# Optimization experiments

Measured on AMD Instinct MI355X. Metric: run time of the kernel, lower is better.

Reference implementation:

```python
import jax, jax.numpy as jnp
import numpy as np

B, N, D, E, H = 8, 256, 128, 32, 4
HD = D // H
EPS = 1e-5


def setup_inputs() -> dict:
    key = jax.random.key(0)
    ks = jax.random.split(key, 20)
    idx = jnp.arange(N)

    h = jax.random.normal(ks[0], (B, N, D), dtype=jnp.float32)
    adj = (jax.random.uniform(ks[1], (B, N, N)) < 0.5).astype(jnp.float32)
    adj = adj.at[:, idx, idx].set(1.0)
    edge_features = jax.random.normal(ks[2], (B, N, N, E), dtype=jnp.float32)
    src_mask = (jax.random.uniform(ks[3], (B, N, N)) < 0.7).astype(jnp.float32)
    src_mask = src_mask.at[:, idx, idx].set(1.0)

    s = 1.0 / np.sqrt(D)
    se = 1.0 / np.sqrt(E)
    p = {
        "gcn_w": jax.random.normal(ks[4], (D, D)) * s,
        "gcn_b": jnp.zeros((D,)),
        "edge_w": jax.random.normal(ks[5], (D, E)) * se,
        "edge_b": jnp.zeros((D,)),
        "wq": jax.random.normal(ks[6], (D, D)) * s,
        "wk": jax.random.normal(ks[7], (D, D)) * s,
        "wv": jax.random.normal(ks[8], (D, D)) * s,
        "bq": jnp.zeros((D,)),
        "bk": jnp.zeros((D,)),
        "bv": jnp.zeros((D,)),
        "out_w": jax.random.normal(ks[9], (D, D)) * s,
        "out_b": jnp.zeros((D,)),
        "ln_g": jnp.ones((D,)),
        "ln_b": jnp.zeros((D,)),
    }
    return {"h": h, "adj": adj, "edge_features": edge_features, "src_mask": src_mask, **p}


def reference(h, adj, edge_features, src_mask,
              gcn_w, gcn_b, edge_w, edge_b,
              wq, wk, wv, bq, bk, bv, out_w, out_b, ln_g, ln_b):
    b, n, d = h.shape

    # --- GCN branch: degree-normalized aggregation with self-loops ---
    adj_sl = adj + jnp.eye(n, dtype=h.dtype)[None]          # (B,N,N)
    deg = adj_sl.sum(-1, keepdims=True)                      # (B,N,1)
    h_agg = jnp.einsum('bnm,bmd->bnd', adj_sl, h) / deg
    h_gcn = h_agg @ gcn_w.T + gcn_b                          # (B,N,D)

    # --- edge-conditioned key/value: h_ij = h_j + edge_emb ---
    edge_emb = jnp.einsum('bnme,de->bnmd', edge_features, edge_w) + edge_b
    h_ij = h[:, None, :, :] + edge_emb                       # (B,N,N,D)

    # key padding mask: True where edge absent (masked)
    masked = (adj * src_mask) == 0                           # (B,N,N)

    # --- multi-head attention, one query per node ---
    q = (h @ wq.T + bq).reshape(b, n, H, HD)                 # (B,N,H,HD)
    k = (jnp.einsum('bnmd,ed->bnme', h_ij, wk) + bk).reshape(b, n, n, H, HD)
    v = (jnp.einsum('bnmd,ed->bnme', h_ij, wv) + bv).reshape(b, n, n, H, HD)

    scores = jnp.einsum('bnhd,bnmhd->bnhm', q, k) / np.sqrt(HD)  # (B,N,H,N)
    scores = jnp.where(masked[:, :, None, :], -jnp.inf, scores)
    attn = jax.nn.softmax(scores, axis=-1)
    o = jnp.einsum('bnhm,bnmhd->bnhd', attn, v).reshape(b, n, d)
    o = o @ out_w.T + out_b                                  # (B,N,D)

    # residual + layernorm (dropout is identity in eval)
    x = h + o
    mu = x.mean(-1, keepdims=True)
    var = ((x - mu) ** 2).mean(-1, keepdims=True)
    h_attn = ln_g * (x - mu) / jnp.sqrt(var + EPS) + ln_b

    return h_gcn + h_attn
```

## Files before the change

### kernel.cpp

```cpp
#include <hip/hip_runtime.h>
#include <hip/hip_bf16.h>

#define OFF_WQT 0
#define OFF_WKT 16384
#define OFF_WVT 32768
#define OFF_OWT 49152
#define OFF_GWT 65536
#define OFF_WKE 81920
#define OFF_WVET 86016
#define OFF_KB  90112
#define OFF_VB  90240
#define OFF_SC  90368
#define OFF_QSP 98560
#define OFF_QEP 229632
#define OFF_HG  360704
#define OFF_K0P 622848
#define OFF_V0P 753920

using half2_t = __attribute__((ext_vector_type(2))) __fp16;

static __device__ __forceinline__ half2_t u2h(unsigned int u){
  union { unsigned int u; half2_t h; } x; x.u = u; return x.h;
}
static __device__ __forceinline__ unsigned int pkf16(float a, float b){
  union { half2_t h; unsigned int u; } x;
  x.h = __builtin_amdgcn_cvt_pkrtz(a, b);
  return x.u;
}
static __device__ __forceinline__ float fdot2(unsigned int a, unsigned int b, float c){
  return __builtin_amdgcn_fdot2(u2h(a), u2h(b), c, false);
}

__global__ __launch_bounds__(256) void prep_kernel(
    const float* __restrict__ wq, const float* __restrict__ wk,
    const float* __restrict__ wv, const float* __restrict__ out_w,
    const float* __restrict__ gcn_w, const float* __restrict__ edge_w,
    const float* __restrict__ edge_b, const float* __restrict__ bk,
    const float* __restrict__ bv, float* __restrict__ ws)
{
  int blk = blockIdx.x, t = threadIdx.x;
  if (blk < 320) {
    int w = blk >> 6;
    int e0 = (blk & 63) * 256 + t;
    const float* src = (w==0) ? wq : (w==1) ? wk : (w==2) ? wv : (w==3) ? out_w : gcn_w;
    float* dst = ws + ((w==0) ? OFF_WQT : (w==1) ? OFF_WKT : (w==2) ? OFF_WVT
                      : (w==3) ? OFF_OWT : OFF_GWT);
    int k = e0 >> 7, d = e0 & 127;
    dst[e0] = src[d*128 + k];
  } else if (blk < 352) {
    int idx = blk - 320;
    int which = idx >> 4;
    int e0 = (idx & 15) * 256 + t;
    int dd = e0 >> 5, e = e0 & 31;
    const float* W = which ? wv : wk;
    float acc = 0.f;
    #pragma unroll 4
    for (int k2 = 0; k2 < 128; ++k2) acc += W[dd*128+k2] * edge_w[k2*32+e];
    if (which) ws[OFF_WVET + e*128 + dd] = acc;
    else       ws[OFF_WKE + e0] = acc;
  } else {
    int dd = t & 127;
    const float* W  = (t < 128) ? wk : wv;
    const float* bb = (t < 128) ? bk : bv;
    float acc = bb[dd];
    #pragma unroll 4
    for (int k2 = 0; k2 < 128; ++k2) acc += W[dd*128+k2] * edge_b[k2];
    ws[((t < 128) ? OFF_KB : OFF_VB) + dd] = acc;
  }
}

__global__ __launch_bounds__(256) void proj_kernel(
    const float* __restrict__ h, const float* __restrict__ adj,
    const float* __restrict__ bq, const float* __restrict__ gcn_b,
    float* __restrict__ ws)
{
  __shared__ float h_lds[256];
  __shared__ float adj_lds[512];
  __shared__ float p1[2][2][128];
  __shared__ float p2[2][2][128];
  __shared__ float p3[2][2][128];
  __shared__ float qrow[2*132];
  __shared__ float qe_l[2*132];
  __shared__ float dpart[2][2];
  __shared__ float ha_lds[2*132];

  int t = threadIdx.x;
  int d = t & 127, kh = t >> 7;
  int r0 = blockIdx.x * 2;
  int b  = r0 >> 8, n0 = r0 & 255;
  unsigned int* wsu = (unsigned int*)ws;

  if (t < 64)  ((float4*)h_lds)[t]   = ((const float4*)(h   + (size_t)r0*128))[t];
  if (t < 128) ((float4*)adj_lds)[t] = ((const float4*)(adj + (size_t)r0*256))[t];
  __syncthreads();

  {
    const float* wqT = ws + OFF_WQT;
    const float* wkT = ws + OFF_WKT;
    const float* wvT = ws + OFF_WVT;
    float aq0=0,aq1=0,ak0=0,ak1=0,av0=0,av1=0;
    #pragma unroll 4
    for (int kk = 0; kk < 64; ++kk) {
      int k = kh*64 + kk;
      float qw = wqT[k*128+d], kw = wkT[k*128+d], vw = wvT[k*128+d];
      float h0 = h_lds[k], h1 = h_lds[128+k];
      aq0 += qw*h0; aq1 += qw*h1;
      ak0 += kw*h0; ak1 += kw*h1;
      av0 += vw*h0; av1 += vw*h1;
    }
    p1[kh][0][d]=aq0; p1[kh][1][d]=aq1;
    p2[kh][0][d]=ak0; p2[kh][1][d]=ak1;
    p3[kh][0][d]=av0; p3[kh][1][d]=av1;
  }
  __syncthreads();

  {
    int i = t >> 7, dd = t & 127;
    const float inv = 0.17677669529663687f;
    qrow[i*132 + dd] = (p1[0][i][dd] + p1[1][i][dd] + bq[dd]) * inv;
  }
  {
    int i = (t >> 6) & 1, pr = t & 63;
    if (t < 128) {
      float k0 = p2[0][i][2*pr] + p2[1][i][2*pr];
      float k1 = p2[0][i][2*pr+1] + p2[1][i][2*pr+1];
      wsu[OFF_K0P + (size_t)(r0+i)*64 + pr] = pkf16(k0, k1);
    } else {
      float v0 = p3[0][i][2*pr] + p3[1][i][2*pr];
      float v1 = p3[0][i][2*pr+1] + p3[1][i][2*pr+1];
      wsu[OFF_V0P + (size_t)(r0+i)*64 + pr] = pkf16(v0, v1);
    }
  }
  __syncthreads();

  if (t < 128) {
    int i = t >> 6, pr = t & 63;
    wsu[OFF_QSP + (size_t)(r0+i)*64 + pr] = pkf16(qrow[i*132 + 2*pr], qrow[i*132 + 2*pr+1]);
  }
  {
    int i = t >> 7, he = t & 127, hh = he >> 5, e = he & 31;
    float acc = 0.f;
    #pragma unroll
    for (int j = 0; j < 32; ++j)
      acc += ws[OFF_WKE + (hh*32 + j)*32 + e] * qrow[i*132 + hh*32 + j];
    qe_l[i*132 + he] = acc;
  }
  if (t < 8) {
    int i = t >> 2, hh = t & 3;
    float acc = 0.f;
    #pragma unroll
    for (int j = 0; j < 32; ++j)
      acc += qrow[i*132 + hh*32 + j] * ws[OFF_KB + hh*32 + j];
    ws[OFF_SC + (size_t)(r0+i)*4 + hh] = acc;
  }
  {
    float ag0=0, ag1=0, dg0=0, dg1=0;
    #pragma unroll 4
    for (int mm = 0; mm < 128; ++mm) {
      int ml = kh*128 + mm;
      float hv = h[((size_t)b*256 + ml)*128 + d];
      float a0 = adj_lds[ml]       + ((ml == n0)     ? 1.0f : 0.0f);
      float a1 = adj_lds[256 + ml] + ((ml == n0 + 1) ? 1.0f : 0.0f);
      ag0 += a0*hv; ag1 += a1*hv; dg0 += a0; dg1 += a1;
    }
    p1[kh][0][d]=ag0; p1[kh][1][d]=ag1;
    if (d == 0) { dpart[kh][0]=dg0; dpart[kh][1]=dg1; }
  }
  __syncthreads();

  if (t < 128) {
    int i = t >> 6, pr = t & 63;
    wsu[OFF_QEP + (size_t)(r0+i)*64 + pr] = pkf16(qe_l[i*132 + 2*pr], qe_l[i*132 + 2*pr+1]);
  }
  {
    int i = t >> 7, dd = t & 127;
    ha_lds[i*132 + dd] = (p1[0][i][dd] + p1[1][i][dd]) / (dpart[0][i] + dpart[1][i]);
  }
  __syncthreads();

  {
    const float* gwT = ws + OFF_GWT;
    float g0=0, g1=0;
    #pragma unroll 4
    for (int kk = 0; kk < 64; ++kk) {
      int k = kh*64 + kk;
      float gw = gwT[k*128+d];
      g0 += gw * ha_lds[k];
      g1 += gw * ha_lds[132 + k];
    }
    p2[kh][0][d]=g0; p2[kh][1][d]=g1;
  }
  __syncthreads();
  {
    int i = t >> 7, dd = t & 127;
    ws[OFF_HG + (size_t)(r0+i)*128 + dd] = p2[0][i][dd] + p2[1][i][dd] + gcn_b[dd];
  }
}

__global__ __launch_bounds__(256, 5) void attn_kernel(
    const float* __restrict__ edge, const float* __restrict__ adj,
    const float* __restrict__ srcm, const float* __restrict__ h,
    const float* __restrict__ out_b, const float* __restrict__ ln_g,
    const float* __restrict__ ln_b, const float* __restrict__ ws,
    float* __restrict__ out)
{
  __shared__ unsigned int e_lds[256*18];
  __shared__ float s_buf[4*264];
  __shared__ float part4[8*132];
  __shared__ float part5[8*132];
  __shared__ float wpart[16];

  float* const s_lds = s_buf;
  float* const eb_l  = s_buf;
  float* const o_l   = s_buf + 132;
  float* const px    = s_buf + 264;
  float* const stat  = s_buf + 520;

  const int t  = threadIdx.x;
  const int bn = blockIdx.x;
  const int b  = bn >> 8;
  const int hh = t & 3;
  const int mq = t >> 2;
  const unsigned int* wsu = (const unsigned int*)ws;

  const float4* et = (const float4*)(edge + (size_t)bn*8192);

  float4 va = et[t];
  float4 vb = et[256 + t];
  float mp_my = adj[(size_t)bn*256 + t] * srcm[(size_t)bn*256 + t];

  unsigned int qs_pk[16], qe_pk[16];
  {
    const uint4* qp = (const uint4*)(wsu + OFF_QSP + (size_t)bn*64 + hh*16);
    const uint4* qe = (const uint4*)(wsu + OFF_QEP + (size_t)bn*64 + hh*16);
    #pragma unroll
    for (int j = 0; j < 4; ++j) {
      uint4 a = qp[j];
      qs_pk[4*j+0]=a.x; qs_pk[4*j+1]=a.y; qs_pk[4*j+2]=a.z; qs_pk[4*j+3]=a.w;
      uint4 c = qe[j];
      qe_pk[4*j+0]=c.x; qe_pk[4*j+1]=c.y; qe_pk[4*j+2]=c.z; qe_pk[4*j+3]=c.w;
    }
  }
  float sconst = ws[OFF_SC + (size_t)bn*4 + hh];
  const unsigned int* K0 = wsu + OFF_K0P + (size_t)b*256*64;

  float exacc = 0.f;
  #pragma unroll
  for (int c = 0; c < 4; ++c) {
    {
      int fi = c*512 + t;
      int row = fi >> 3, c4 = fi & 7;
      uint2 pk;
      pk.x = pkf16(va.x, va.y);
      pk.y = pkf16(va.z, va.w);
      *(uint2*)(e_lds + row*18 + c4*2) = pk;
      int fj = fi + 256;
      int row2 = fj >> 3, c42 = fj & 7;
      uint2 pk2;
      pk2.x = pkf16(vb.x, vb.y);
      pk2.y = pkf16(vb.z, vb.w);
      *(uint2*)(e_lds + row2*18 + c42*2) = pk2;
    }
    if (c == 0) e_lds[t*18 + 16] = __float_as_uint(mp_my);
    if (c < 3) {
      va = et[(c+1)*512 + t];
      vb = et[(c+1)*512 + 256 + t];
    }
    __syncthreads();

    int mm = (c << 6) | mq;
    float acc = sconst;
    const uint4* kr4 = (const uint4*)(K0 + (size_t)mm*64 + hh*16);
    #pragma unroll
    for (int j4 = 0; j4 < 4; ++j4) {
      uint4 kw = kr4[j4];
      acc = fdot2(qs_pk[4*j4+0], kw.x, acc);
      acc = fdot2(qs_pk[4*j4+1], kw.y, acc);
      acc = fdot2(qs_pk[4*j4+2], kw.z, acc);
      acc = fdot2(qs_pk[4*j4+3], kw.w, acc);
    }
    const uint2* er = (const uint2*)(e_lds + mm*18);
    #pragma unroll
    for (int j2 = 0; j2 < 8; ++j2) {
      uint2 w = er[j2];
      acc = fdot2(qe_pk[2*j2+0], w.x, acc);
      acc = fdot2(qe_pk[2*j2+1], w.y, acc);
    }
    float mp = __uint_as_float(e_lds[mm*18 + 16]);
    float ex = (mp == 0.0f) ? 0.0f : __expf(acc);
    s_lds[hh*264 + mm] = ex;
    exacc += ex;
  }
  exacc += __shfl_down(exacc, 4);
  exacc += __shfl_down(exacc, 8);
  exacc += __shfl_down(exacc, 16);
  exacc += __shfl_down(exacc, 32);
  if ((t & 63) < 4) wpart[(t >> 6)*4 + hh] = exacc;
  __syncthreads();

  {
    int ms  = t >> 5;
    int hh4 = (t >> 3) & 3, e4 = t & 7;
    int c   = t & 31,  hh5 = c >> 3;
    float p4x=0,p4y=0,p4z=0,p4w=0;
    float p5x=0,p5y=0,p5z=0,p5w=0;
    const unsigned int* vrow = wsu + OFF_V0P + (size_t)b*256*64;
    for (int jm = 0; jm < 32; ++jm) {
      int mm = ms*32 + jm;
      float a4 = s_lds[hh4*264 + mm];
      uint2 w = *(const uint2*)(e_lds + mm*18 + e4*2);
      half2_t e0 = u2h(w.x), e1 = u2h(w.y);
      p4x += a4*(float)e0.x; p4y += a4*(float)e0.y;
      p4z += a4*(float)e1.x; p4w += a4*(float)e1.y;
      float a5 = s_lds[hh5*264 + mm];
      uint2 vv = *(const uint2*)(vrow + (size_t)mm*64 + c*2);
      half2_t v0 = u2h(vv.x), v1 = u2h(vv.y);
      p5x += a5*(float)v0.x; p5y += a5*(float)v0.y;
      p5z += a5*(float)v1.x; p5w += a5*(float)v1.y;
    }
    float4 f4; f4.x=p4x; f4.y=p4y; f4.z=p4z; f4.w=p4w;
    *(float4*)(part4 + ms*132 + hh4*32 + e4*4) = f4;
    float4 f5; f5.x=p5x; f5.y=p5y; f5.z=p5z; f5.w=p5w;
    *(float4*)(part5 + ms*132 + c*4) = f5;
  }
  __syncthreads();

  float ov_reg = 0.f;
  if (t < 128) {
    int ht = t >> 5;
    float inv = 1.0f / (wpart[ht] + wpart[4+ht] + wpart[8+ht] + wpart[12+ht]);
    float se = 0.f, s2 = 0.f;
    #pragma unroll
    for (int g = 0; g < 8; ++g) { se += part4[g*132 + t]; s2 += part5[g*132 + t]; }
    eb_l[t] = se * inv;
    ov_reg  = s2 * inv;
  }
  __syncthreads();

  if (t < 128) {
    int hd = t >> 5;
    float acc = ov_reg + ws[OFF_VB + t];
    const float* wveT = ws + OFF_WVET;
    #pragma unroll 4
    for (int e = 0; e < 32; ++e) acc += wveT[e*128 + t] * eb_l[hd*32 + e];
    o_l[t] = acc;
  }
  __syncthreads();

  {
    int d = t & 127, kh = t >> 7;
    const float* owT = ws + OFF_OWT;
    float xa = 0.f;
    #pragma unroll 4
    for (int kk = 0; kk < 64; ++kk) {
      int k = kh*64 + kk;
      xa += owT[k*128 + d] * o_l[k];
    }
    px[kh*128 + d] = xa;
  }
  __syncthreads();

  float x = 0.f;
  if (t < 128) {
    x = px[t] + px[128 + t] + out_b[t] + h[(size_t)bn*128 + t];
    float s = x, ss = x*x;
    #pragma unroll
    for (int off = 32; off > 0; off >>= 1) {
      s  += __shfl_down(s,  off);
      ss += __shfl_down(ss, off);
    }
    if ((t & 63) == 0) { stat[t >> 6] = s; stat[2 + (t >> 6)] = ss; }
  }
  __syncthreads();

  if (t < 128) {
    float mu   = (stat[0] + stat[1]) * (1.0f/128.0f);
    float var  = (stat[2] + stat[3]) * (1.0f/128.0f) - mu*mu;
    float rstd = rsqrtf(var + 1e-5f);
    out[(size_t)bn*128 + t] =
        ln_g[t]*(x - mu)*rstd + ln_b[t] + ws[OFF_HG + (size_t)bn*128 + t];
  }
}

extern "C" void kernel_launch(void* const* d_in, const int* in_sizes, int n_in,
                              void* d_out, int out_size, void* d_ws, size_t ws_size,
                              hipStream_t stream) {
  (void)in_sizes; (void)n_in; (void)out_size; (void)ws_size;
  const float* h     = (const float*)d_in[0];
  const float* adj   = (const float*)d_in[1];
  const float* edge  = (const float*)d_in[2];
  const float* srcm  = (const float*)d_in[3];
  const float* gcn_w = (const float*)d_in[4];
  const float* gcn_b = (const float*)d_in[5];
  const float* edge_w= (const float*)d_in[6];
  const float* edge_b= (const float*)d_in[7];
  const float* wq    = (const float*)d_in[8];
  const float* wk    = (const float*)d_in[9];
  const float* wv    = (const float*)d_in[10];
  const float* bq    = (const float*)d_in[11];
  const float* bk    = (const float*)d_in[12];
  const float* bv    = (const float*)d_in[13];
  const float* out_w = (const float*)d_in[14];
  const float* out_b = (const float*)d_in[15];
  const float* ln_g  = (const float*)d_in[16];
  const float* ln_b  = (const float*)d_in[17];

  float* ws  = (float*)d_ws;
  float* out = (float*)d_out;

  prep_kernel<<<353, 256, 0, stream>>>(wq, wk, wv, out_w, gcn_w, edge_w, edge_b, bk, bv, ws);
  proj_kernel<<<1024, 256, 0, stream>>>(h, adj, bq, gcn_b, ws);
  attn_kernel<<<2048, 256, 0, stream>>>(edge, adj, srcm, h, out_b, ln_g, ln_b, ws, out);
}
```

Measured before the change: 185.4 us.

## Stream edge chunks through double-buffered LDS and fuse weighted sums per chunk

Replaces the full 256-row edge LDS tile and the partial-sum buffers with a double-buffered 64-row chunk buffer. The attention-weighted edge and value sums are now accumulated chunk by chunk, split across the two thread halves. This shrinks shared memory so the launch bound can rise from 5 to 8 blocks per CU. It also prefetches h and the GCN output early. In exchange it adds a barrier per chunk, leaves half the threads idle-imbalanced in each chunk phase, and uses a less vectorized LDS access pattern.

```diff
diff --git a/kernel.cpp b/kernel.cpp
--- a/kernel.cpp
+++ b/kernel.cpp
@@ -197,24 +197,22 @@
   }
 }
 
-__global__ __launch_bounds__(256, 5) void attn_kernel(
+__global__ __launch_bounds__(256, 8) void attn_kernel(
     const float* __restrict__ edge, const float* __restrict__ adj,
     const float* __restrict__ srcm, const float* __restrict__ h,
     const float* __restrict__ out_b, const float* __restrict__ ln_g,
     const float* __restrict__ ln_b, const float* __restrict__ ws,
     float* __restrict__ out)
 {
-  __shared__ unsigned int e_lds[256*18];
-  __shared__ float s_buf[4*264];
-  __shared__ float part4[8*132];
-  __shared__ float part5[8*132];
+  __shared__ unsigned int e_buf[2*64*18];
+  __shared__ float s_chunk[4*66];
   __shared__ float wpart[16];
-
-  float* const s_lds = s_buf;
-  float* const eb_l  = s_buf;
-  float* const o_l   = s_buf + 132;
-  float* const px    = s_buf + 264;
-  float* const stat  = s_buf + 520;
+  __shared__ float ovh[128];
+  __shared__ float eb_l[128];
+  __shared__ float ov_l[128];
+  __shared__ float o_l[128];
+  __shared__ float px[256];
+  __shared__ float stat[4];
 
   const int t  = threadIdx.x;
   const int bn = blockIdx.x;
@@ -227,7 +225,10 @@
 
   float4 va = et[t];
   float4 vb = et[256 + t];
-  float mp_my = adj[(size_t)bn*256 + t] * srcm[(size_t)bn*256 + t];
+  float mp0 = adj[(size_t)bn*256 +       mq] * srcm[(size_t)bn*256 +       mq];
+  float mp1 = adj[(size_t)bn*256 +  64 + mq] * srcm[(size_t)bn*256 +  64 + mq];
+  float mp2 = adj[(size_t)bn*256 + 128 + mq] * srcm[(size_t)bn*256 + 128 + mq];
+  float mp3 = adj[(size_t)bn*256 + 192 + mq] * srcm[(size_t)bn*256 + 192 + mq];
 
   unsigned int qs_pk[16], qe_pk[16];
   {
@@ -244,104 +245,125 @@
   float sconst = ws[OFF_SC + (size_t)bn*4 + hh];
   const unsigned int* K0 = wsu + OFF_K0P + (size_t)b*256*64;
 
+  float h_pre = 0.f, hg_pre = 0.f;
+  if (t < 128) {
+    h_pre  = h[(size_t)bn*128 + t];
+    hg_pre = ws[OFF_HG + (size_t)bn*128 + t];
+  }
+
   float exacc = 0.f;
+  float acc4 = 0.f;
+  float acc5x = 0.f, acc5y = 0.f;
+
   #pragma unroll
   for (int c = 0; c < 4; ++c) {
+    unsigned int* eb = e_buf + (c & 1)*64*18;
     {
-      int fi = c*512 + t;
-      int row = fi >> 3, c4 = fi & 7;
+      int lr = t >> 3, c4 = t & 7;
       uint2 pk;
-      pk.x = pkf16(va.x, va.y);
-      pk.y = pkf16(va.z, va.w);
-      *(uint2*)(e_lds + row*18 + c4*2) = pk;
-      int fj = fi + 256;
-      int row2 = fj >> 3, c42 = fj & 7;
+      pk.x = pkf16(va.x, va.y); pk.y = pkf16(va.z, va.w);
+      *(uint2*)(eb + lr*18 + c4*2) = pk;
       uint2 pk2;
-      pk2.x = pkf16(vb.x, vb.y);
-      pk2.y = pkf16(vb.z, vb.w);
-      *(uint2*)(e_lds + row2*18 + c42*2) = pk2;
-    }
-    if (c == 0) e_lds[t*18 + 16] = __float_as_uint(mp_my);
+      pk2.x = pkf16(vb.x, vb.y); pk2.y = pkf16(vb.z, vb.w);
+      *(uint2*)(eb + (32 + lr)*18 + c4*2) = pk2;
+    }
     if (c < 3) {
       va = et[(c+1)*512 + t];
       vb = et[(c+1)*512 + 256 + t];
     }
     __syncthreads();
 
-    int mm = (c << 6) | mq;
-    float acc = sconst;
-    const uint4* kr4 = (const uint4*)(K0 + (size_t)mm*64 + hh*16);
-    #pragma unroll
-    for (int j4 = 0; j4 < 4; ++j4) {
-      uint4 kw = kr4[j4];
-      acc = fdot2(qs_pk[4*j4+0], kw.x, acc);
-      acc = fdot2(qs_pk[4*j4+1], kw.y, acc);
-      acc = fdot2(qs_pk[4*j4+2], kw.z, acc);
-      acc = fdot2(qs_pk[4*j4+3], kw.w, acc);
-    }
-    const uint2* er = (const uint2*)(e_lds + mm*18);
-    #pragma unroll
-    for (int j2 = 0; j2 < 8; ++j2) {
-      uint2 w = er[j2];
-      acc = fdot2(qe_pk[2*j2+0], w.x, acc);
-      acc = fdot2(qe_pk[2*j2+1], w.y, acc);
-    }
-    float mp = __uint_as_float(e_lds[mm*18 + 16]);
-    float ex = (mp == 0.0f) ? 0.0f : __expf(acc);
-    s_lds[hh*264 + mm] = ex;
-    exacc += ex;
-  }
+    {
+      int gm = c*64 + mq;
+      float acc = sconst;
+      const uint4* kr4 = (const uint4*)(K0 + (size_t)gm*64 + hh*16);
+      #pragma unroll
+      for (int j4 = 0; j4 < 4; ++j4) {
+        uint4 kw = kr4[j4];
+        acc = fdot2(qs_pk[4*j4+0], kw.x, acc);
+        acc = fdot2(qs_pk[4*j4+1], kw.y, acc);
+        acc = fdot2(qs_pk[4*j4+2], kw.z, acc);
+        acc = fdot2(qs_pk[4*j4+3], kw.w, acc);
+      }
+      const uint2* er = (const uint2*)(eb + mq*18);
+      #pragma unroll
+      for (int j2 = 0; j2 < 8; ++j2) {
+        uint2 w = er[j2];
+        acc = fdot2(qe_pk[2*j2+0], w.x, acc);
+        acc = fdot2(qe_pk[2*j2+1], w.y, acc);
+      }
+      float mp = (c==0) ? mp0 : (c==1) ? mp1 : (c==2) ? mp2 : mp3;
+      float ex = (mp == 0.0f) ? 0.0f : __expf(acc);
+      s_chunk[hh*66 + mq] = ex;
+      exacc += ex;
+    }
+    __syncthreads();
+
+    if (t < 128) {
+      int e = t & 31, ht = t >> 5;
+      const float* sc_ = s_chunk + ht*66;
+      const unsigned int* ebr = eb + (e >> 1);
+      bool hi = (e & 1);
+      float a0 = 0.f, a1 = 0.f;
+      #pragma unroll 8
+      for (int m = 0; m < 64; m += 2) {
+        float s0 = sc_[m], s1 = sc_[m+1];
+        half2_t w0 = u2h(ebr[m*18]);
+        half2_t w1 = u2h(ebr[(m+1)*18]);
+        float e0 = hi ? (float)w0.y : (float)w0.x;
+        float e1 = hi ? (float)w1.y : (float)w1.x;
+        a0 += s0*e0; a1 += s1*e1;
+      }
+      acc4 += a0 + a1;
+    } else {
+      int idx = t - 128;
+      int j = idx & 63, mh = idx >> 6;
+      int head = j >> 4;
+      const float* sc_ = s_chunk + head*66 + mh*32;
+      const unsigned int* vp = wsu + OFF_V0P + ((size_t)b*256 + c*64 + mh*32)*64 + j;
+      float a0 = 0.f, a1 = 0.f;
+      #pragma unroll 8
+      for (int m = 0; m < 32; ++m) {
+        float s = sc_[m];
+        half2_t v = u2h(vp[(size_t)m*64]);
+        a0 += s*(float)v.x; a1 += s*(float)v.y;
+      }
+      acc5x += a0; acc5y += a1;
+    }
+  }
+
   exacc += __shfl_down(exacc, 4);
   exacc += __shfl_down(exacc, 8);
   exacc += __shfl_down(exacc, 16);
   exacc += __shfl_down(exacc, 32);
   if ((t & 63) < 4) wpart[(t >> 6)*4 + hh] = exacc;
-  __syncthreads();
-
-  {
-    int ms  = t >> 5;
-    int hh4 = (t >> 3) & 3, e4 = t & 7;
-    int c   = t & 31,  hh5 = c >> 3;
-    float p4x=0,p4y=0,p4z=0,p4w=0;
-    float p5x=0,p5y=0,p5z=0,p5w=0;
-    const unsigned int* vrow = wsu + OFF_V0P + (size_t)b*256*64;
-    for (int jm = 0; jm < 32; ++jm) {
-      int mm = ms*32 + jm;
-      float a4 = s_lds[hh4*264 + mm];
-      uint2 w = *(const uint2*)(e_lds + mm*18 + e4*2);
-      half2_t e0 = u2h(w.x), e1 = u2h(w.y);
-      p4x += a4*(float)e0.x; p4y += a4*(float)e0.y;
-      p4z += a4*(float)e1.x; p4w += a4*(float)e1.y;
-      float a5 = s_lds[hh5*264 + mm];
-      uint2 vv = *(const uint2*)(vrow + (size_t)mm*64 + c*2);
-      half2_t v0 = u2h(vv.x), v1 = u2h(vv.y);
-      p5x += a5*(float)v0.x; p5y += a5*(float)v0.y;
-      p5z += a5*(float)v1.x; p5w += a5*(float)v1.y;
-    }
-    float4 f4; f4.x=p4x; f4.y=p4y; f4.z=p4z; f4.w=p4w;
-    *(float4*)(part4 + ms*132 + hh4*32 + e4*4) = f4;
-    float4 f5; f5.x=p5x; f5.y=p5y; f5.z=p5z; f5.w=p5w;
-    *(float4*)(part5 + ms*132 + c*4) = f5;
-  }
-  __syncthreads();
-
-  float ov_reg = 0.f;
+  if (t >= 192) {
+    int j = (t - 128) & 63;
+    float2 p; p.x = acc5x; p.y = acc5y;
+    *(float2*)(ovh + j*2) = p;
+  }
+  __syncthreads();
+
   if (t < 128) {
     int ht = t >> 5;
     float inv = 1.0f / (wpart[ht] + wpart[4+ht] + wpart[8+ht] + wpart[12+ht]);
-    float se = 0.f, s2 = 0.f;
-    #pragma unroll
-    for (int g = 0; g < 8; ++g) { se += part4[g*132 + t]; s2 += part5[g*132 + t]; }
-    eb_l[t] = se * inv;
-    ov_reg  = s2 * inv;
+    eb_l[t] = acc4 * inv;
+  } else if (t < 192) {
+    int j = t - 128, head = j >> 4;
+    float inv = 1.0f / (wpart[head] + wpart[4+head] + wpart[8+head] + wpart[12+head]);
+    float2 oh = *(const float2*)(ovh + j*2);
+    float2 res;
+    res.x = (acc5x + oh.x)*inv + ws[OFF_VB + 2*j];
+    res.y = (acc5y + oh.y)*inv + ws[OFF_VB + 2*j + 1];
+    *(float2*)(ov_l + 2*j) = res;
   }
   __syncthreads();
 
   if (t < 128) {
     int hd = t >> 5;
-    float acc = ov_reg + ws[OFF_VB + t];
+    float acc = ov_l[t];
     const float* wveT = ws + OFF_WVET;
-    #pragma unroll 4
+    #pragma unroll 8
     for (int e = 0; e < 32; ++e) acc += wveT[e*128 + t] * eb_l[hd*32 + e];
     o_l[t] = acc;
   }
@@ -351,7 +373,7 @@
     int d = t & 127, kh = t >> 7;
     const float* owT = ws + OFF_OWT;
     float xa = 0.f;
-    #pragma unroll 4
+    #pragma unroll 8
     for (int kk = 0; kk < 64; ++kk) {
       int k = kh*64 + kk;
       xa += owT[k*128 + d] * o_l[k];
@@ -362,7 +384,7 @@
 
   float x = 0.f;
   if (t < 128) {
-    x = px[t] + px[128 + t] + out_b[t] + h[(size_t)bn*128 + t];
+    x = px[t] + px[128 + t] + out_b[t] + h_pre;
     float s = x, ss = x*x;
     #pragma unroll
     for (int off = 32; off > 0; off >>= 1) {
@@ -378,7 +400,7 @@
     float var  = (stat[2] + stat[3]) * (1.0f/128.0f) - mu*mu;
     float rstd = rsqrtf(var + 1e-5f);
     out[(size_t)bn*128 + t] =
-        ln_g[t]*(x - mu)*rstd + ln_b[t] + ws[OFF_HG + (size_t)bn*128 + t];
+        ln_g[t]*(x - mu)*rstd + ln_b[t] + hg_pre;
   }
 }
 
```

New measurement: 227.5 us. 22.7% more time.
